# Performance work log

Measured on AMD Instinct MI355X. Metric: run time of the kernel, lower is better.

The kernel has to match this reference:

```python
import jax, jax.numpy as jnp
import numpy as np
import math

D_MODEL = 2048
D_QK = 128
D_V = 128
SEQ = 4096

def setup_inputs() -> dict:
    key = jax.random.key(0)
    ks = jax.random.split(key, 9)
    s = 1.0 / math.sqrt(D_MODEL)
    return {
        "input_q": jax.random.normal(ks[0], (SEQ, D_MODEL), jnp.float32),
        "input_k": jax.random.normal(ks[1], (SEQ, D_MODEL), jnp.float32),
        "input_v": jax.random.normal(ks[2], (SEQ, D_MODEL), jnp.float32),
        "WQ_w": jax.random.normal(ks[3], (D_QK, D_MODEL), jnp.float32) * s,
        "WQ_b": jax.random.normal(ks[4], (D_QK,), jnp.float32) * s,
        "WK_w": jax.random.normal(ks[5], (D_QK, D_MODEL), jnp.float32) * s,
        "WK_b": jax.random.normal(ks[6], (D_QK,), jnp.float32) * s,
        "WV_w": jax.random.normal(ks[7], (D_V, D_MODEL), jnp.float32) * s,
        "WV_b": jax.random.normal(ks[8], (D_V,), jnp.float32) * s,
    }

def reference(input_q, input_k, input_v, WQ_w, WQ_b, WK_w, WK_b, WV_w, WV_b):
    # Linear projections (torch nn.Linear: x @ W.T + b)
    Q = input_q @ WQ_w.T + WQ_b   # [S, d_qk]
    K = input_k @ WK_w.T + WK_b   # [S, d_qk]
    V = input_v @ WV_w.T + WV_b   # [S, d_v]
    S = Q.shape[0]
    # causal mask: -inf strictly above the diagonal, 0 elsewhere
    mask = jnp.triu(jnp.full((S, S), -jnp.inf, dtype=Q.dtype), k=1)
    # NOTE: original code adds mask BEFORE dividing by sqrt(d_model)
    scores = (Q @ K.T + mask) / math.sqrt(D_MODEL)  # [S, S]
    attn = jax.nn.softmax(scores, axis=-1)
    return attn @ V  # [S, d_v]
```

## Files before the change

kernel.cpp:

```cpp
#include <hip/hip_runtime.h>

#define SEQ 4096
#define DM  2048
#define DH  128
#define NSPLIT 8

typedef __attribute__((ext_vector_type(8))) short bf16x8;
typedef __attribute__((ext_vector_type(4))) short short4v;
typedef __attribute__((ext_vector_type(4))) float f32x4;

__device__ inline short f2bf(float f) {
    union { float f; unsigned u; } x; x.f = f;
    unsigned r = x.u + 0x7fffu + ((x.u >> 16) & 1u);
    return (short)(r >> 16);
}

__device__ inline float fexp2(float f) { return __builtin_amdgcn_exp2f(f); }

__device__ inline void lds_barrier() {
    asm volatile("s_waitcnt lgkmcnt(0)\n\ts_barrier" ::: "memory");
}

__global__ __launch_bounds__(256) void convw_kernel(
    const float* __restrict__ wq, const float* __restrict__ wk, const float* __restrict__ wv,
    short* __restrict__ Wbf)
{
    int idx = blockIdx.x * 256 + threadIdx.x;
    int mat = idx >> 16;
    int off = (idx & 65535) * 4;
    const float* W = (mat == 0) ? wq : (mat == 1) ? wk : wv;
    float4 v = *reinterpret_cast<const float4*>(W + off);
    short4v s = { f2bf(v.x), f2bf(v.y), f2bf(v.z), f2bf(v.w) };
    *reinterpret_cast<short4v*>(Wbf + (size_t)mat * DH * DM + off) = s;
}

__global__ __launch_bounds__(256) void proj_kernel(
    const float* __restrict__ inq, const float* __restrict__ ink, const float* __restrict__ inv,
    const short* __restrict__ Wbf,
    float* __restrict__ Pqk, float* __restrict__ Pv)
{
    const int mat = blockIdx.y;
    const int s   = blockIdx.z;
    const float* A = (mat == 0) ? inq : (mat == 1) ? ink : inv;

    const int tid  = threadIdx.x;
    const int lane = tid & 63;
    const int w    = tid >> 6;
    const int g    = lane >> 4;
    const int c16  = lane & 15;
    const int i0   = blockIdx.x * 64;
    const int kb   = s * 512;

    __shared__ short Alds[64][72];
    __shared__ short Wlds[128][72];

    const int ar = tid >> 2, ac = (tid & 3) * 16;
    const float* Aload = A + (size_t)(i0 + ar) * DM + kb + ac;
    const int wr = tid >> 1, wc = (tid & 1) * 32;
    const short* Wload = Wbf + (size_t)mat * DH * DM + (size_t)wr * DM + kb + wc;

    f32x4 acc[2][4];
    #pragma unroll
    for (int mI = 0; mI < 2; mI++)
        #pragma unroll
        for (int n = 0; n < 4; n++) acc[mI][n] = (f32x4){0.f, 0.f, 0.f, 0.f};

    float4  abuf[4][4];
    bf16x8  wbuf[2][4];

    #pragma unroll
    for (int d = 0; d < 2; d++) {
        #pragma unroll
        for (int j = 0; j < 4; j++)
            wbuf[d][j] = *reinterpret_cast<const bf16x8*>(Wload + d * 64 + j * 8);
        #pragma unroll
        for (int j = 0; j < 4; j++)
            abuf[d][j] = *reinterpret_cast<const float4*>(Aload + d * 64 + j * 4);
    }
    #pragma unroll
    for (int d = 2; d < 4; d++)
        #pragma unroll
        for (int j = 0; j < 4; j++)
            abuf[d][j] = *reinterpret_cast<const float4*>(Aload + d * 64 + j * 4);

    const int rw = (w >> 1) * 32;
    const int cw = (w & 1) * 64;

    #pragma unroll
    for (int c = 0; c < 8; c++) {
        const int da = c & 3, dw = c & 1;
        {
            #pragma unroll
            for (int j = 0; j < 4; j++)
                *reinterpret_cast<bf16x8*>(&Wlds[wr][wc + j * 8]) = wbuf[dw][j];
            #pragma unroll
            for (int j = 0; j < 2; j++) {
                float4 v0 = abuf[da][j * 2], v1 = abuf[da][j * 2 + 1];
                bf16x8 sv = { f2bf(v0.x), f2bf(v0.y), f2bf(v0.z), f2bf(v0.w),
                              f2bf(v1.x), f2bf(v1.y), f2bf(v1.z), f2bf(v1.w) };
                *reinterpret_cast<bf16x8*>(&Alds[ar][ac + j * 8]) = sv;
            }
        }
        if (c + 2 < 8) {
            #pragma unroll
            for (int j = 0; j < 4; j++)
                wbuf[dw][j] = *reinterpret_cast<const bf16x8*>(Wload + (c + 2) * 64 + j * 8);
        }
        if (c + 4 < 8) {
            #pragma unroll
            for (int j = 0; j < 4; j++)
                abuf[da][j] = *reinterpret_cast<const float4*>(Aload + (c + 4) * 64 + j * 4);
        }
        lds_barrier();
        #pragma unroll
        for (int kk = 0; kk < 2; kk++) {
            bf16x8 af0 = *reinterpret_cast<const bf16x8*>(&Alds[rw + c16][kk * 32 + g * 8]);
            bf16x8 af1 = *reinterpret_cast<const bf16x8*>(&Alds[rw + 16 + c16][kk * 32 + g * 8]);
            #pragma unroll
            for (int n = 0; n < 4; n++) {
                bf16x8 wf = *reinterpret_cast<const bf16x8*>(
                    &Wlds[cw + n * 16 + c16][kk * 32 + g * 8]);
                acc[0][n] = __builtin_amdgcn_mfma_f32_16x16x32_bf16(af0, wf, acc[0][n], 0, 0, 0);
                acc[1][n] = __builtin_amdgcn_mfma_f32_16x16x32_bf16(af1, wf, acc[1][n], 0, 0, 0);
            }
        }
        lds_barrier();
    }

    if (mat < 2) {
        float* outp = Pqk + ((size_t)(mat * 4 + s) * SEQ) * DH;
        #pragma unroll
        for (int mI = 0; mI < 2; mI++) {
            int row0 = i0 + rw + mI * 16 + g * 4;
            #pragma unroll
            for (int n = 0; n < 4; n++) {
                int col = cw + n * 16 + c16;
                #pragma unroll
                for (int r = 0; r < 4; r++)
                    outp[(size_t)(row0 + r) * DH + col] = acc[mI][n][r];
            }
        }
    } else {
        float* outp = Pv + (size_t)s * DH * SEQ;
        #pragma unroll
        for (int mI = 0; mI < 2; mI++) {
            int row0 = i0 + rw + mI * 16 + g * 4;
            #pragma unroll
            for (int n = 0; n < 4; n++) {
                int col = cw + n * 16 + c16;
                float4 f = { acc[mI][n][0], acc[mI][n][1], acc[mI][n][2], acc[mI][n][3] };
                *reinterpret_cast<float4*>(&outp[(size_t)col * SEQ + row0]) = f;
            }
        }
    }
}

__global__ __launch_bounds__(256) void combine_kernel(
    const float* __restrict__ Pqk, const float* __restrict__ Pv,
    const float* __restrict__ bq, const float* __restrict__ bk, const float* __restrict__ bv,
    short* __restrict__ Qws, short* __restrict__ Kws, short* __restrict__ Vtws)
{
    const int b = blockIdx.x;
    if (b < 1024) {
        int tid = b * 256 + threadIdx.x;
        int mat = tid >> 17;
        int idx4 = (tid & 131071) * 4;
        float4 acc = {0.f, 0.f, 0.f, 0.f};
        #pragma unroll
        for (int s = 0; s < 4; s++) {
            float4 p = *reinterpret_cast<const float4*>(
                Pqk + ((size_t)(mat * 4 + s) * SEQ) * DH + idx4);
            acc.x += p.x; acc.y += p.y; acc.z += p.z; acc.w += p.w;
        }
        const float* bias = (mat == 0) ? bq : bk;
        int col = idx4 & (DH - 1);
        acc.x += bias[col]; acc.y += bias[col + 1]; acc.z += bias[col + 2]; acc.w += bias[col + 3];
        short4v o = { f2bf(acc.x), f2bf(acc.y), f2bf(acc.z), f2bf(acc.w) };
        short* outp = (mat == 0) ? Qws : Kws;
        *reinterpret_cast<short4v*>(outp + idx4) = o;
    } else {
        int tid = (b - 1024) * 256 + threadIdx.x;
        int idx4 = tid * 4;
        float4 acc = {0.f, 0.f, 0.f, 0.f};
        #pragma unroll
        for (int s = 0; s < 4; s++) {
            float4 p = *reinterpret_cast<const float4*>(Pv + (size_t)s * DH * SEQ + idx4);
            acc.x += p.x; acc.y += p.y; acc.z += p.z; acc.w += p.w;
        }
        float bvv = bv[idx4 >> 12];
        acc.x += bvv; acc.y += bvv; acc.z += bvv; acc.w += bvv;
        short4v o = { f2bf(acc.x), f2bf(acc.y), f2bf(acc.z), f2bf(acc.w) };
        *reinterpret_cast<short4v*>(Vtws + idx4) = o;
    }
}

__global__ __launch_bounds__(256) void flash_kernel(
    const short* __restrict__ Qws, const short* __restrict__ Kws, const short* __restrict__ Vtws,
    float* __restrict__ Opart, float* __restrict__ mpart, float* __restrict__ lpart)
{
    const int bid = blockIdx.x;
    const int y   = bid >> 6;
    const int qbr = bid & 63;
    const int qb  = (y >= 4) ? (63 - qbr) : qbr;
    const int tid = threadIdx.x;
    const int w    = tid >> 6;
    const int lane = tid & 63;
    const int g = lane >> 4, c16 = lane & 15;
    const int i0 = qb * 64 + w * 16;

    __shared__ short Klds[64][136];
    __shared__ short Vlds[128][72];
    __shared__ short Slds[4][16][72];

    const int kkey = tid >> 2,  kdim = (tid & 3) * 32;
    const int vdim = tid >> 1,  vkey = (tid & 1) * 32;

    bf16x8 kreg[4], vreg[4];

    bf16x8 qf[4];
    #pragma unroll
    for (int kk = 0; kk < 4; kk++)
        qf[kk] = *reinterpret_cast<const bf16x8*>(Qws + (size_t)(i0 + c16) * DH + kk * 32 + g * 8);

    float m[4], lsum[4];
    f32x4 O[8];
    #pragma unroll
    for (int r = 0; r < 4; r++) { m[r] = -__builtin_inff(); lsum[r] = 0.f; }
    #pragma unroll
    for (int c = 0; c < 8; c++) O[c] = (f32x4){0.f, 0.f, 0.f, 0.f};

    const float C = 0.03188448666f;

    if (qb >= y) {
        {
            const int j0 = y * 64;
            #pragma unroll
            for (int j = 0; j < 4; j++) {
                kreg[j] = *reinterpret_cast<const bf16x8*>(
                    Kws + (size_t)(j0 + kkey) * DH + kdim + j * 8);
                vreg[j] = *reinterpret_cast<const bf16x8*>(
                    Vtws + (size_t)vdim * SEQ + j0 + vkey + j * 8);
            }
            #pragma unroll
            for (int j = 0; j < 4; j++) {
                *reinterpret_cast<bf16x8*>(&Klds[kkey][kdim + j * 8]) = kreg[j];
                *reinterpret_cast<bf16x8*>(&Vlds[vdim][vkey + j * 8]) = vreg[j];
            }
        }
        lds_barrier();

        for (int jt = y; jt <= qb; jt += NSPLIT) {
            const bool more = (jt + NSPLIT <= qb);
            if (more) {
                const int jn = (jt + NSPLIT) * 64;
                #pragma unroll
                for (int j = 0; j < 4; j++) {
                    kreg[j] = *reinterpret_cast<const bf16x8*>(
                        Kws + (size_t)(jn + kkey) * DH + kdim + j * 8);
                    vreg[j] = *reinterpret_cast<const bf16x8*>(
                        Vtws + (size_t)vdim * SEQ + jn + vkey + j * 8);
                }
            }
            const int j0 = jt * 64;
            f32x4 S[4];
            #pragma unroll
            for (int t = 0; t < 4; t++) S[t] = (f32x4){0.f, 0.f, 0.f, 0.f};
            __builtin_amdgcn_s_setprio(1);
            #pragma unroll
            for (int kk = 0; kk < 4; kk++) {
                #pragma unroll
                for (int t = 0; t < 4; t++) {
                    bf16x8 kf = *reinterpret_cast<const bf16x8*>(
                        &Klds[t * 16 + c16][kk * 32 + g * 8]);
                    S[t] = __builtin_amdgcn_mfma_f32_16x16x32_bf16(qf[kk], kf, S[t], 0, 0, 0);
                }
            }
            __builtin_amdgcn_s_setprio(0);
            float s2[4][4];
            #pragma unroll
            for (int t = 0; t < 4; t++) {
                int key = j0 + t * 16 + c16;
                #pragma unroll
                for (int r = 0; r < 4; r++) {
                    int q = i0 + g * 4 + r;
                    s2[t][r] = (key > q) ? -__builtin_inff() : S[t][r] * C;
                }
            }
            float mnew[4], alpha[4];
            #pragma unroll
            for (int r = 0; r < 4; r++) {
                float rm = fmaxf(fmaxf(s2[0][r], s2[1][r]), fmaxf(s2[2][r], s2[3][r]));
                rm = fmaxf(rm, __shfl_xor(rm, 1));
                rm = fmaxf(rm, __shfl_xor(rm, 2));
                rm = fmaxf(rm, __shfl_xor(rm, 4));
                rm = fmaxf(rm, __shfl_xor(rm, 8));
                mnew[r] = fmaxf(m[r], rm);
                alpha[r] = fexp2(m[r] - mnew[r]);
                m[r] = mnew[r];
            }
            #pragma unroll
            for (int r = 0; r < 4; r++) {
                float ps = 0.f;
                #pragma unroll
                for (int t = 0; t < 4; t++) {
                    float p = fexp2(s2[t][r] - mnew[r]);
                    ps += p;
                    Slds[w][g * 4 + r][t * 16 + c16] = f2bf(p);
                }
                ps += __shfl_xor(ps, 1);
                ps += __shfl_xor(ps, 2);
                ps += __shfl_xor(ps, 4);
                ps += __shfl_xor(ps, 8);
                lsum[r] = lsum[r] * alpha[r] + ps;
                #pragma unroll
                for (int c = 0; c < 8; c++) O[c][r] *= alpha[r];
            }
            __builtin_amdgcn_s_setprio(1);
            #pragma unroll
            for (int kk2 = 0; kk2 < 2; kk2++) {
                bf16x8 pf = *reinterpret_cast<const bf16x8*>(&Slds[w][c16][kk2 * 32 + g * 8]);
                #pragma unroll
                for (int c = 0; c < 8; c++) {
                    bf16x8 vf = *reinterpret_cast<const bf16x8*>(
                        &Vlds[c * 16 + c16][kk2 * 32 + g * 8]);
                    O[c] = __builtin_amdgcn_mfma_f32_16x16x32_bf16(pf, vf, O[c], 0, 0, 0);
                }
            }
            __builtin_amdgcn_s_setprio(0);
            lds_barrier();
            if (more) {
                #pragma unroll
                for (int j = 0; j < 4; j++) {
                    *reinterpret_cast<bf16x8*>(&Klds[kkey][kdim + j * 8]) = kreg[j];
                    *reinterpret_cast<bf16x8*>(&Vlds[vdim][vkey + j * 8]) = vreg[j];
                }
                lds_barrier();
            }
        }
        #pragma unroll
        for (int c = 0; c < 8; c++) {
            int col = c * 16 + c16;
            #pragma unroll
            for (int r = 0; r < 4; r++)
                Opart[((size_t)y * SEQ + i0 + g * 4 + r) * DH + col] = O[c][r];
        }
    }
    if (c16 == 0) {
        #pragma unroll
        for (int r = 0; r < 4; r++) {
            mpart[y * SEQ + i0 + g * 4 + r] = m[r];
            lpart[y * SEQ + i0 + g * 4 + r] = lsum[r];
        }
    }
}

__global__ __launch_bounds__(256) void merge_kernel(
    const float* __restrict__ Opart, const float* __restrict__ mpart, const float* __restrict__ lpart,
    float* __restrict__ out, int NS)
{
    const int row = blockIdx.x * 2 + (threadIdx.x >> 7);
    const int col = threadIdx.x & 127;
    float mh[16];
    float M = -__builtin_inff();
    for (int hh = 0; hh < NS; hh++) {
        mh[hh] = mpart[hh * SEQ + row];
        M = fmaxf(M, mh[hh]);
    }
    float denom = 0.f, num = 0.f;
    for (int hh = 0; hh < NS; hh++) {
        float wgt = fexp2(mh[hh] - M);
        denom += lpart[hh * SEQ + row] * wgt;
        num   += Opart[((size_t)hh * SEQ + row) * DH + col] * wgt;
    }
    out[(size_t)row * DH + col] = num / denom;
}

extern "C" void kernel_launch(void* const* d_in, const int* in_sizes, int n_in,
                              void* d_out, int out_size, void* d_ws, size_t ws_size,
                              hipStream_t stream) {
    const float* inq = (const float*)d_in[0];
    const float* ink = (const float*)d_in[1];
    const float* inv = (const float*)d_in[2];
    const float* wq  = (const float*)d_in[3];
    const float* bq  = (const float*)d_in[4];
    const float* wk  = (const float*)d_in[5];
    const float* bk  = (const float*)d_in[6];
    const float* wv  = (const float*)d_in[7];
    const float* bv  = (const float*)d_in[8];

    char* ws = (char*)d_ws;
    short* Qws   = (short*)(ws);
    short* Kws   = (short*)(ws + (1u << 20));
    short* Vtws  = (short*)(ws + (2u << 20));
    short* Wbf   = (short*)(ws + (3u << 20));
    float* Pqk   = (float*)(ws + 4718592);
    float* Pv    = (float*)(ws + 21495808);
    float* Opart = (float*)(ws + (3u << 20));
    float* mpart = (float*)(ws + (3u << 20) + (size_t)NSPLIT * SEQ * DH * 4);
    float* lpart = mpart + (size_t)NSPLIT * SEQ;

    convw_kernel<<<768, 256, 0, stream>>>(wq, wk, wv, Wbf);
    proj_kernel<<<dim3(64, 3, 4), 256, 0, stream>>>(inq, ink, inv, Wbf, Pqk, Pv);
    combine_kernel<<<1536, 256, 0, stream>>>(Pqk, Pv, bq, bk, bv, Qws, Kws, Vtws);
    flash_kernel<<<512, 256, 0, stream>>>(Qws, Kws, Vtws, Opart, mpart, lpart);
    merge_kernel<<<2048, 256, 0, stream>>>(Opart, mpart, lpart, (float*)d_out, NSPLIT);
}
```

Before: 180.2 us.

## Stage projection tiles with direct global-to-LDS loads and XOR swizzle

The projection GEMM now moves A (fp32) and W (bf16) tiles straight from global memory into double-buffered LDS with global_load_lds, instead of going through registers. It applies an XOR swizzle to avoid bank conflicts. The fp32-to-bf16 conversion of A now happens after the LDS read rather than before the LDS write, and raw vmcnt waits pipeline the next stage behind the current MFMAs. This cuts VGPR pressure and register-staged copies. In exchange LDS use grows, since A is stored as fp32 in two buffers, and A is converted redundantly by both column-half waves.

Measured after the change: 182.3 us. Within noise of the previous version (+1.2%).

```diff
diff --git a/kernel.cpp b/kernel.cpp
--- a/kernel.cpp
+++ b/kernel.cpp
@@ -19,6 +19,12 @@
 
 __device__ inline void lds_barrier() {
     asm volatile("s_waitcnt lgkmcnt(0)\n\ts_barrier" ::: "memory");
+}
+
+__device__ inline void gload16(const void* g, void* l) {
+    __builtin_amdgcn_global_load_lds(
+        (const __attribute__((address_space(1))) unsigned int*)g,
+        (__attribute__((address_space(3))) unsigned int*)l, 16, 0, 0);
 }
 
 __global__ __launch_bounds__(256) void convw_kernel(
@@ -51,13 +57,20 @@
     const int i0   = blockIdx.x * 64;
     const int kb   = s * 512;
 
-    __shared__ short Alds[64][72];
-    __shared__ short Wlds[128][72];
-
-    const int ar = tid >> 2, ac = (tid & 3) * 16;
-    const float* Aload = A + (size_t)(i0 + ar) * DM + kb + ac;
-    const int wr = tid >> 1, wc = (tid & 1) * 32;
-    const short* Wload = Wbf + (size_t)mat * DH * DM + (size_t)wr * DM + kb + wc;
+    __shared__ float Alds[2][64][64];
+    __shared__ short Wlds[2][128][64];
+
+    const int arow = lane >> 4;
+    const float* pA0 = A + (size_t)(i0 + w * 16 + 0 + arow) * DM + kb
+                         + (size_t)(((lane & 15) ^ arow) << 2);
+    const float* pA1 = A + (size_t)(i0 + w * 16 + 4 + arow) * DM + kb
+                         + (size_t)(((lane & 15) ^ (4 + arow)) << 2);
+    const int wrow = lane >> 3;
+    const short* pW = Wbf + (size_t)mat * DH * DM + (size_t)(w * 32 + wrow) * DM + kb
+                          + (size_t)(((lane & 7) ^ wrow) << 3);
+
+    char* aldsw = (char*)&Alds[0][0][0] + w * 4096;
+    char* wldsw = (char*)&Wlds[0][0][0] + w * 4096;
 
     f32x4 acc[2][4];
     #pragma unroll
@@ -65,67 +78,70 @@
         #pragma unroll
         for (int n = 0; n < 4; n++) acc[mI][n] = (f32x4){0.f, 0.f, 0.f, 0.f};
 
-    float4  abuf[4][4];
-    bf16x8  wbuf[2][4];
-
-    #pragma unroll
-    for (int d = 0; d < 2; d++) {
-        #pragma unroll
-        for (int j = 0; j < 4; j++)
-            wbuf[d][j] = *reinterpret_cast<const bf16x8*>(Wload + d * 64 + j * 8);
-        #pragma unroll
-        for (int j = 0; j < 4; j++)
-            abuf[d][j] = *reinterpret_cast<const float4*>(Aload + d * 64 + j * 4);
-    }
-    #pragma unroll
-    for (int d = 2; d < 4; d++)
-        #pragma unroll
-        for (int j = 0; j < 4; j++)
-            abuf[d][j] = *reinterpret_cast<const float4*>(Aload + d * 64 + j * 4);
-
     const int rw = (w >> 1) * 32;
     const int cw = (w & 1) * 64;
 
+    #define STAGE(cc, b) do {                                                  \
+        const float* a_ = pA0 + (cc) * 64;                                     \
+        const float* a2_ = pA1 + (cc) * 64;                                    \
+        const short* w_ = pW + (cc) * 64;                                      \
+        char* al_ = aldsw + (b) * 16384;                                       \
+        char* wl_ = wldsw + (b) * 16384;                                       \
+        gload16(a_,            al_);                                           \
+        gload16(a2_,           al_ + 1024);                                    \
+        gload16(a_  + 8 * DM,  al_ + 2048);                                    \
+        gload16(a2_ + 8 * DM,  al_ + 3072);                                    \
+        gload16(w_,            wl_);                                           \
+        gload16(w_ + 8 * DM,   wl_ + 1024);                                    \
+        gload16(w_ + 16 * DM,  wl_ + 2048);                                    \
+        gload16(w_ + 24 * DM,  wl_ + 3072);                                    \
+    } while (0)
+
+    STAGE(0, 0);
+
     #pragma unroll
     for (int c = 0; c < 8; c++) {
-        const int da = c & 3, dw = c & 1;
-        {
-            #pragma unroll
-            for (int j = 0; j < 4; j++)
-                *reinterpret_cast<bf16x8*>(&Wlds[wr][wc + j * 8]) = wbuf[dw][j];
-            #pragma unroll
-            for (int j = 0; j < 2; j++) {
-                float4 v0 = abuf[da][j * 2], v1 = abuf[da][j * 2 + 1];
-                bf16x8 sv = { f2bf(v0.x), f2bf(v0.y), f2bf(v0.z), f2bf(v0.w),
-                              f2bf(v1.x), f2bf(v1.y), f2bf(v1.z), f2bf(v1.w) };
-                *reinterpret_cast<bf16x8*>(&Alds[ar][ac + j * 8]) = sv;
-            }
-        }
-        if (c + 2 < 8) {
-            #pragma unroll
-            for (int j = 0; j < 4; j++)
-                wbuf[dw][j] = *reinterpret_cast<const bf16x8*>(Wload + (c + 2) * 64 + j * 8);
-        }
-        if (c + 4 < 8) {
-            #pragma unroll
-            for (int j = 0; j < 4; j++)
-                abuf[da][j] = *reinterpret_cast<const float4*>(Aload + (c + 4) * 64 + j * 4);
-        }
-        lds_barrier();
+        if (c + 1 < 8) {
+            STAGE(c + 1, (c + 1) & 1);
+            asm volatile("s_waitcnt vmcnt(8)" ::: "memory");
+        } else {
+            asm volatile("s_waitcnt vmcnt(0)" ::: "memory");
+        }
+        asm volatile("s_barrier" ::: "memory");
+        const int b = c & 1;
         #pragma unroll
         for (int kk = 0; kk < 2; kk++) {
-            bf16x8 af0 = *reinterpret_cast<const bf16x8*>(&Alds[rw + c16][kk * 32 + g * 8]);
-            bf16x8 af1 = *reinterpret_cast<const bf16x8*>(&Alds[rw + 16 + c16][kk * 32 + g * 8]);
+            bf16x8 af0, af1;
+            {
+                const int row = rw + c16;
+                const int cu0 = (kk * 8 + g * 2) ^ (row & 7);
+                const int cu1 = (kk * 8 + g * 2 + 1) ^ (row & 7);
+                float4 lo = *reinterpret_cast<const float4*>(&Alds[b][row][cu0 << 2]);
+                float4 hi = *reinterpret_cast<const float4*>(&Alds[b][row][cu1 << 2]);
+                af0 = (bf16x8){ f2bf(lo.x), f2bf(lo.y), f2bf(lo.z), f2bf(lo.w),
+                                f2bf(hi.x), f2bf(hi.y), f2bf(hi.z), f2bf(hi.w) };
+            }
+            {
+                const int row = rw + 16 + c16;
+                const int cu0 = (kk * 8 + g * 2) ^ (row & 7);
+                const int cu1 = (kk * 8 + g * 2 + 1) ^ (row & 7);
+                float4 lo = *reinterpret_cast<const float4*>(&Alds[b][row][cu0 << 2]);
+                float4 hi = *reinterpret_cast<const float4*>(&Alds[b][row][cu1 << 2]);
+                af1 = (bf16x8){ f2bf(lo.x), f2bf(lo.y), f2bf(lo.z), f2bf(lo.w),
+                                f2bf(hi.x), f2bf(hi.y), f2bf(hi.z), f2bf(hi.w) };
+            }
             #pragma unroll
             for (int n = 0; n < 4; n++) {
-                bf16x8 wf = *reinterpret_cast<const bf16x8*>(
-                    &Wlds[cw + n * 16 + c16][kk * 32 + g * 8]);
+                const int col = cw + n * 16 + c16;
+                const int up  = (kk * 4 + g) ^ (col & 7);
+                bf16x8 wf = *reinterpret_cast<const bf16x8*>(&Wlds[b][col][up << 3]);
                 acc[0][n] = __builtin_amdgcn_mfma_f32_16x16x32_bf16(af0, wf, acc[0][n], 0, 0, 0);
                 acc[1][n] = __builtin_amdgcn_mfma_f32_16x16x32_bf16(af1, wf, acc[1][n], 0, 0, 0);
             }
         }
         lds_barrier();
     }
+    #undef STAGE
 
     if (mat < 2) {
         float* outp = Pqk + ((size_t)(mat * 4 + s) * SEQ) * DH;
```
